# Kernel tuning notes

Hardware: AMD Instinct MI355X
Metric: run time of the kernel (lower is better)

The kernel has to match this reference:

```python
import jax, jax.numpy as jnp
import numpy as np
from jax import lax

B, T, D = 8, 4096, 1024


def setup_inputs() -> dict:
    key = jax.random.key(0)
    ks = jax.random.split(key, 8)
    s = 1.0 / np.sqrt(D)  # keep GEMM outputs O(1)
    return {
        "x": jax.random.normal(ks[0], (B, T, D), dtype=jnp.float32),
        "state_p": jnp.zeros((B, D), dtype=jnp.float32),
        "decay": 0.8 + 0.19 * jax.random.uniform(ks[1], (D,), dtype=jnp.float32),  # ~0.9, stable
        "mass": jnp.ones((D,), dtype=jnp.float32),
        "Wq": s * jax.random.normal(ks[2], (D, D), dtype=jnp.float32),
        "bq": jnp.zeros((D,), dtype=jnp.float32),
        "Wk": s * jax.random.normal(ks[3], (D, D), dtype=jnp.float32),
        "bk": jnp.zeros((D,), dtype=jnp.float32),
        "Wv": s * jax.random.normal(ks[4], (D, D), dtype=jnp.float32),
        "bv": jnp.zeros((D,), dtype=jnp.float32),
    }


def reference(x, state_p, decay, mass, Wq, bq, Wk, bk, Wv, bv):
    # Batch all per-timestep projections into single GEMMs over (B*T) tokens.
    k_logit = jnp.einsum("btd,ed->bte", x, Wk) + bk        # [B,T,D]
    v = jnp.einsum("btd,ed->bte", x, Wv) + bv              # [B,T,D]
    u = jax.nn.sigmoid(k_logit) * v                          # gated input, [B,T,D]

    # Diagonal linear recurrence p_t = decay * p_{t-1} + u_t via scan over time.
    def step(p, u_t):
        p = p * decay + u_t
        return p, p

    final_p, ps = lax.scan(step, state_p, jnp.swapaxes(u, 0, 1))  # ps: [T,B,D]
    p = jnp.swapaxes(ps, 0, 1)                                     # [B,T,D]

    velocities = (jnp.einsum("btd,ed->bte", p, Wq) + bq) / mass    # [B,T,D]
    return velocities, final_p
```

## Files before the change

### kernel.cpp

```cpp
#include <hip/hip_runtime.h>
#include <stdint.h>
#include <stddef.h>

#define D_DIM 1024
#define T_LEN 4096
#define B_SZ 8
#define M_ROWS 32768
#define KTOT 1024
#define CHUNK 64
#define NCHUNK 64

typedef unsigned short u16;
typedef unsigned short u16x8 __attribute__((ext_vector_type(8)));
typedef __bf16 bf16x8 __attribute__((ext_vector_type(8)));
typedef float f32x4 __attribute__((ext_vector_type(4)));

__device__ __forceinline__ u16 f2bf(float f) {
    union { float f; unsigned u; } v; v.f = f;
    unsigned r = v.u + 0x7fffu + ((v.u >> 16) & 1u);
    return (u16)(r >> 16);
}
__device__ __forceinline__ float bf2f(u16 h) {
    union { unsigned u; float f; } v; v.u = ((unsigned)h) << 16;
    return v.f;
}

__global__ void convert_all_kernel(const float* __restrict__ x,
                                   const float* __restrict__ Wk, const float* __restrict__ Wv,
                                   const float* __restrict__ Wq,
                                   u16* __restrict__ xb, u16* __restrict__ wcat,
                                   u16* __restrict__ wqb) {
    const int NX = (M_ROWS * D_DIM) / 4;
    const int total = NX + 3072 * 256;
    int stride = gridDim.x * blockDim.x;
    for (int j = blockIdx.x * blockDim.x + threadIdx.x; j < total; j += stride) {
        const float4* s4;
        ushort4* d4;
        if (j < NX) {
            s4 = (const float4*)x + j;
            d4 = (ushort4*)xb + j;
        } else {
            int idx = j - NX;
            int r = idx >> 8, c4 = idx & 255;
            if (r < 2048) {
                int g = r >> 5, jj = r & 31;
                s4 = (const float4*)((jj < 16 ? Wk : Wv) + (size_t)(g * 16 + (jj & 15)) * D_DIM) + c4;
                d4 = (ushort4*)(wcat + (size_t)r * D_DIM) + c4;
            } else {
                s4 = (const float4*)(Wq + (size_t)(r - 2048) * D_DIM) + c4;
                d4 = (ushort4*)(wqb + (size_t)(r - 2048) * D_DIM) + c4;
            }
        }
        float4 v = *s4;
        ushort4 o;
        o.x = f2bf(v.x); o.y = f2bf(v.y); o.z = f2bf(v.z); o.w = f2bf(v.w);
        *d4 = o;
    }
}

__device__ __forceinline__ void gload16(const u16* g, u16* l) {
    __builtin_amdgcn_global_load_lds(
        (const __attribute__((address_space(1))) void*)g,
        (__attribute__((address_space(3))) void*)l,
        16, 0, 0);
}

template<bool CAT>
__global__ __launch_bounds__(512, 2) void gemm18_kernel(
    const u16* __restrict__ A,
    const u16* __restrict__ Bg,
    const float* __restrict__ bias0,
    const float* __restrict__ bias1,
    u16* __restrict__ Uout,
    float* __restrict__ Fout,
    const float* __restrict__ decay,
    float* __restrict__ localc)
{
    constexpr int NT = KTOT / 64;
    __shared__ u16 smem[2 * 32768];

    const int tid  = threadIdx.x;
    const int w    = tid >> 6;
    const int lane = tid & 63;

    const int cpx = gridDim.x >> 3;
    const int swz = (blockIdx.x & 7) * cpx + (blockIdx.x >> 3);
    const int nCol = CAT ? 8 : 4;
    const int M0 = (swz / nCol) * 256;
    const int N0 = (swz % nCol) * 256;

    const int srow = lane >> 2;
    const int sg   = (lane & 3) ^ ((srow >> 1) & 3);

    const u16* pA0 = A  + (size_t)(M0 + w * 32 +      srow) * KTOT + sg * 8;
    const u16* pA1 = A  + (size_t)(M0 + w * 32 + 16 + srow) * KTOT + sg * 8;
    const u16* pB0 = Bg + (size_t)(N0 + w * 32 +      srow) * KTOT + sg * 8;
    const u16* pB1 = Bg + (size_t)(N0 + w * 32 + 16 + srow) * KTOT + sg * 8;

    auto stA = [&](u16* nxt, int h) {
        gload16(pA0, nxt + h * 8192 + w * 1024);       pA0 += 32;
        gload16(pA1, nxt + h * 8192 + w * 1024 + 512); pA1 += 32;
    };
    auto stB = [&](u16* nxt, int h) {
        gload16(pB0, nxt + 16384 + h * 8192 + w * 1024);       pB0 += 32;
        gload16(pB1, nxt + 16384 + h * 8192 + w * 1024 + 512); pB1 += 32;
    };

    const int wrow = (w >> 2) * 128;
    const int wcol = (w & 3) * 64;
    const int fr = lane & 15;
    const int fq = lane >> 4;

    int offA[8], offB[4];
#pragma unroll
    for (int m = 0; m < 8; ++m) {
        int row = wrow + m * 16 + fr;
        offA[m] = row * 32 + ((fq ^ ((row >> 1) & 3)) << 3);
    }
#pragma unroll
    for (int n = 0; n < 4; ++n) {
        int row = wcol + n * 16 + fr;
        offB[n] = 16384 + row * 32 + ((fq ^ ((row >> 1) & 3)) << 3);
    }

    f32x4 acc[8][4] = {};
    bf16x8 aA[4], aB[4], aC[4], aD[4], bA[4], bC[4];

    stA(smem, 0); stB(smem, 0); stA(smem, 1); stB(smem, 1);
    asm volatile("s_waitcnt vmcnt(4)" ::: "memory");
    __builtin_amdgcn_s_barrier();
#pragma unroll
    for (int m = 0; m < 4; ++m) aA[m] = *(const bf16x8*)(smem + offA[m]);
#pragma unroll
    for (int n = 0; n < 4; ++n) bA[n] = *(const bf16x8*)(smem + offB[n]);

#pragma unroll 1
    for (int t = 0; t < NT; ++t) {
        const u16* cur = smem + (t & 1) * 32768;
        u16* nxt = smem + ((t + 1) & 1) * 32768;
        const bool pf = (t + 1 < NT);

#pragma unroll
        for (int m = 0; m < 4; ++m) aB[m] = *(const bf16x8*)(cur + offA[4 + m]);
        if (pf) stA(nxt, 0);
#pragma unroll
        for (int m = 0; m < 4; ++m)
#pragma unroll
            for (int n = 0; n < 4; ++n)
                acc[m][n] = __builtin_amdgcn_mfma_f32_16x16x32_bf16(aA[m], bA[n], acc[m][n], 0, 0, 0);

        if (pf) { asm volatile("s_waitcnt vmcnt(2)" ::: "memory"); }
        else    { asm volatile("s_waitcnt vmcnt(0)" ::: "memory"); }
        __builtin_amdgcn_s_barrier();
#pragma unroll
        for (int m = 0; m < 4; ++m) aC[m] = *(const bf16x8*)(cur + 8192 + offA[m]);
#pragma unroll
        for (int n = 0; n < 4; ++n) bC[n] = *(const bf16x8*)(cur + 8192 + offB[n]);
        if (pf) stB(nxt, 0);
#pragma unroll
        for (int m = 0; m < 4; ++m)
#pragma unroll
            for (int n = 0; n < 4; ++n)
                acc[4 + m][n] = __builtin_amdgcn_mfma_f32_16x16x32_bf16(aB[m], bA[n], acc[4 + m][n], 0, 0, 0);

#pragma unroll
        for (int m = 0; m < 4; ++m) aD[m] = *(const bf16x8*)(cur + 8192 + offA[4 + m]);
        if (pf) stA(nxt, 1);
#pragma unroll
        for (int m = 0; m < 4; ++m)
#pragma unroll
            for (int n = 0; n < 4; ++n)
                acc[m][n] = __builtin_amdgcn_mfma_f32_16x16x32_bf16(aC[m], bC[n], acc[m][n], 0, 0, 0);

        if (pf) { asm volatile("s_waitcnt vmcnt(2)" ::: "memory"); }
        __builtin_amdgcn_s_barrier();
        if (pf) {
#pragma unroll
            for (int m = 0; m < 4; ++m) aA[m] = *(const bf16x8*)(nxt + offA[m]);
#pragma unroll
            for (int n = 0; n < 4; ++n) bA[n] = *(const bf16x8*)(nxt + offB[n]);
            stB(nxt, 1);
        }
#pragma unroll
        for (int m = 0; m < 4; ++m)
#pragma unroll
            for (int n = 0; n < 4; ++n)
                acc[4 + m][n] = __builtin_amdgcn_mfma_f32_16x16x32_bf16(aD[m], bC[n], acc[4 + m][n], 0, 0, 0);
    }

    if (CAT) {
        asm volatile("s_waitcnt lgkmcnt(0) vmcnt(0)" ::: "memory");
        __syncthreads();
        u16 (*uld)[128] = (u16(*)[128])smem;
        const int ucol0 = N0 / 2;
#pragma unroll
        for (int m = 0; m < 8; ++m) {
#pragma unroll
            for (int p = 0; p < 2; ++p) {
                int lcol = (w & 3) * 32 + p * 16 + fr;
                float b0 = bias0[ucol0 + lcol];
                float b1 = bias1[ucol0 + lcol];
#pragma unroll
                for (int j = 0; j < 4; ++j) {
                    int row = wrow + m * 16 + fq * 4 + j;
                    float kl = acc[m][2 * p][j] + b0;
                    float vv = acc[m][2 * p + 1][j] + b1;
                    float sig = 1.0f / (1.0f + __expf(-kl));
                    uld[row][lcol ^ (((row >> 2) & 3) << 4)] = f2bf(sig * vv);
                }
            }
        }
        __syncthreads();
#pragma unroll
        for (int g = 0; g < 8; ++g) {
            int idx = tid + g * 512;
            int row = idx >> 4, grp = idx & 15;
            int lcol = (grp * 8) ^ (((row >> 2) & 3) << 4);
            *(u16x8*)(Uout + (size_t)(M0 + row) * D_DIM + ucol0 + grp * 8) =
                *(const u16x8*)&uld[row][lcol];
        }
        {
            int chunk = tid >> 7;
            int col   = tid & 127;
            float dec = decay[ucol0 + col];
            float carry = 0.f;
#pragma unroll 4
            for (int s = 0; s < 64; ++s) {
                int r = chunk * 64 + s;
                carry = fmaf(carry, dec, bf2f(uld[r][col ^ (((r >> 2) & 3) << 4)]));
            }
            localc[(size_t)(M0 / 64 + chunk) * D_DIM + ucol0 + col] = carry;
        }
    } else {
#pragma unroll
        for (int n = 0; n < 4; ++n) {
            int col = N0 + wcol + n * 16 + fr;
            float b0 = bias0[col];
            float b1 = bias1[col];
#pragma unroll
            for (int m = 0; m < 8; ++m) {
                int row0 = M0 + wrow + m * 16 + fq * 4;
#pragma unroll
                for (int j = 0; j < 4; ++j)
                    Fout[(size_t)(row0 + j) * D_DIM + col] = (acc[m][n][j] + b0) / b1;
            }
        }
    }
}

__global__ __launch_bounds__(1024) void carry_scan_kernel(
    const float* __restrict__ localc, const float* __restrict__ state_p,
    const float* __restrict__ decay, float* __restrict__ prefix,
    float* __restrict__ final_p)
{
    __shared__ float Vs[64][17], Gs[64][17];
    const int tid = threadIdx.x;
    const int c  = tid >> 4;
    const int dl = tid & 15;
    const int b  = blockIdx.x >> 6;
    const int dg = blockIdx.x & 63;
    const int d  = dg * 16 + dl;

    float dec = decay[d];
    float g = dec;
#pragma unroll
    for (int i = 0; i < 6; ++i) g *= g;
    float v = localc[(size_t)(b * NCHUNK + c) * D_DIM + d];
    Vs[c][dl] = v; Gs[c][dl] = g;
    __syncthreads();
#pragma unroll
    for (int s = 1; s < 64; s <<= 1) {
        float lv = 0.f, lg = 1.f;
        if (c >= s) { lv = Vs[c - s][dl]; lg = Gs[c - s][dl]; }
        __syncthreads();
        if (c >= s) {
            float sv = Vs[c][dl], sgg = Gs[c][dl];
            Vs[c][dl] = fmaf(lv, sgg, sv);
            Gs[c][dl] = lg * sgg;
        }
        __syncthreads();
    }
    float P0 = state_p[b * D_DIM + d];
    float pref = (c == 0) ? P0 : fmaf(P0, Gs[c - 1][dl], Vs[c - 1][dl]);
    prefix[(size_t)(b * NCHUNK + c) * D_DIM + d] = pref;
    if (c == 63)
        final_p[b * D_DIM + d] = fmaf(P0, Gs[63][dl], Vs[63][dl]);
}

__global__ void reconstruct_kernel(u16* __restrict__ u, const float* __restrict__ decay,
                                   const float* __restrict__ prefix) {
    int id = blockIdx.x * blockDim.x + threadIdx.x;
    int d8 = id & 127;
    int c  = (id >> 7) & (NCHUNK - 1);
    int b  = id >> 13;
    float4 dlo = ((const float4*)decay)[d8 * 2];
    float4 dhi = ((const float4*)decay)[d8 * 2 + 1];
    float dec[8] = {dlo.x, dlo.y, dlo.z, dlo.w, dhi.x, dhi.y, dhi.z, dhi.w};
    const float* pf = prefix + ((size_t)(b * NCHUNK + c)) * D_DIM + d8 * 8;
    float p[8];
#pragma unroll
    for (int j = 0; j < 8; ++j) p[j] = pf[j];
    u16* up = u + ((size_t)b * T_LEN + (size_t)c * CHUNK) * D_DIM + d8 * 8;
    for (int s = 0; s < CHUNK; ++s) {
        u16x8 v = *(const u16x8*)(up + (size_t)s * D_DIM);
        u16x8 o;
#pragma unroll
        for (int j = 0; j < 8; ++j) {
            p[j] = fmaf(p[j], dec[j], bf2f(v[j]));
            o[j] = f2bf(p[j]);
        }
        *(u16x8*)(up + (size_t)s * D_DIM) = o;
    }
}

extern "C" void kernel_launch(void* const* d_in, const int* in_sizes, int n_in,
                              void* d_out, int out_size, void* d_ws, size_t ws_size,
                              hipStream_t stream) {
    const float* x       = (const float*)d_in[0];
    const float* state_p = (const float*)d_in[1];
    const float* decay   = (const float*)d_in[2];
    const float* mass    = (const float*)d_in[3];
    const float* Wq      = (const float*)d_in[4];
    const float* bq      = (const float*)d_in[5];
    const float* Wk      = (const float*)d_in[6];
    const float* bk      = (const float*)d_in[7];
    const float* Wv      = (const float*)d_in[8];
    const float* bv      = (const float*)d_in[9];

    float* out     = (float*)d_out;
    float* final_p = out + (size_t)M_ROWS * D_DIM;

    u16* xb = (u16*)d_out;

    u16* wcat = (u16*)d_ws;
    u16* wqb  = wcat + 2048 * 1024;
    u16* ub   = wqb + 1024 * 1024;
    float* localc = (float*)(ub + (size_t)M_ROWS * D_DIM);
    float* prefix = localc + B_SZ * NCHUNK * D_DIM;

    convert_all_kernel<<<4096, 256, 0, stream>>>(x, Wk, Wv, Wq, xb, wcat, wqb);

    gemm18_kernel<true><<<dim3(1024), dim3(512), 0, stream>>>(
        xb, wcat, bk, bv, ub, nullptr, decay, localc);

    carry_scan_kernel<<<512, 1024, 0, stream>>>(localc, state_p, decay, prefix, final_p);
    reconstruct_kernel<<<256, 256, 0, stream>>>(ub, decay, prefix);

    gemm18_kernel<false><<<dim3(512), dim3(512), 0, stream>>>(
        ub, wqb, bq, mass, nullptr, out, nullptr, nullptr);
}
```

Before: 291.7 us.

## Split final Wq GEMM into dedicated 256x128-tile kernel with 1024 blocks

```diff
diff --git a/kernel.cpp b/kernel.cpp
--- a/kernel.cpp
+++ b/kernel.cpp
@@ -65,14 +65,12 @@
         16, 0, 0);
 }
 
-template<bool CAT>
-__global__ __launch_bounds__(512, 2) void gemm18_kernel(
+__global__ __launch_bounds__(512, 2) void gemm_cat_kernel(
     const u16* __restrict__ A,
     const u16* __restrict__ Bg,
     const float* __restrict__ bias0,
     const float* __restrict__ bias1,
     u16* __restrict__ Uout,
-    float* __restrict__ Fout,
     const float* __restrict__ decay,
     float* __restrict__ localc)
 {
@@ -85,9 +83,8 @@
 
     const int cpx = gridDim.x >> 3;
     const int swz = (blockIdx.x & 7) * cpx + (blockIdx.x >> 3);
-    const int nCol = CAT ? 8 : 4;
-    const int M0 = (swz / nCol) * 256;
-    const int N0 = (swz % nCol) * 256;
+    const int M0 = (swz >> 3) * 256;
+    const int N0 = (swz & 7) * 256;
 
     const int srow = lane >> 2;
     const int sg   = (lane & 3) ^ ((srow >> 1) & 3);
@@ -107,7 +104,6 @@
     };
 
     const int wrow = (w >> 2) * 128;
-    const int wcol = (w & 3) * 64;
     const int fr = lane & 15;
     const int fq = lane >> 4;
 
@@ -119,7 +115,7 @@
     }
 #pragma unroll
     for (int n = 0; n < 4; ++n) {
-        int row = wcol + n * 16 + fr;
+        int row = (w & 3) * 64 + n * 16 + fr;
         offB[n] = 16384 + row * 32 + ((fq ^ ((row >> 1) & 3)) << 3);
     }
 
@@ -188,62 +184,149 @@
                 acc[4 + m][n] = __builtin_amdgcn_mfma_f32_16x16x32_bf16(aD[m], bC[n], acc[4 + m][n], 0, 0, 0);
     }
 
-    if (CAT) {
-        asm volatile("s_waitcnt lgkmcnt(0) vmcnt(0)" ::: "memory");
-        __syncthreads();
-        u16 (*uld)[128] = (u16(*)[128])smem;
-        const int ucol0 = N0 / 2;
-#pragma unroll
-        for (int m = 0; m < 8; ++m) {
-#pragma unroll
-            for (int p = 0; p < 2; ++p) {
-                int lcol = (w & 3) * 32 + p * 16 + fr;
-                float b0 = bias0[ucol0 + lcol];
-                float b1 = bias1[ucol0 + lcol];
-#pragma unroll
-                for (int j = 0; j < 4; ++j) {
-                    int row = wrow + m * 16 + fq * 4 + j;
-                    float kl = acc[m][2 * p][j] + b0;
-                    float vv = acc[m][2 * p + 1][j] + b1;
-                    float sig = 1.0f / (1.0f + __expf(-kl));
-                    uld[row][lcol ^ (((row >> 2) & 3) << 4)] = f2bf(sig * vv);
-                }
+    asm volatile("s_waitcnt lgkmcnt(0) vmcnt(0)" ::: "memory");
+    __syncthreads();
+
+    u16 (*uld)[128] = (u16(*)[128])smem;
+    const int ucol0 = N0 / 2;
+#pragma unroll
+    for (int m = 0; m < 8; ++m) {
+#pragma unroll
+        for (int p = 0; p < 2; ++p) {
+            int lcol = (w & 3) * 32 + p * 16 + fr;
+            float b0 = bias0[ucol0 + lcol];
+            float b1 = bias1[ucol0 + lcol];
+#pragma unroll
+            for (int j = 0; j < 4; ++j) {
+                int row = wrow + m * 16 + fq * 4 + j;
+                float kl = acc[m][2 * p][j] + b0;
+                float vv = acc[m][2 * p + 1][j] + b1;
+                float sig = 1.0f / (1.0f + __expf(-kl));
+                uld[row][lcol ^ (((row >> 2) & 3) << 4)] = f2bf(sig * vv);
             }
         }
-        __syncthreads();
-#pragma unroll
-        for (int g = 0; g < 8; ++g) {
-            int idx = tid + g * 512;
-            int row = idx >> 4, grp = idx & 15;
-            int lcol = (grp * 8) ^ (((row >> 2) & 3) << 4);
-            *(u16x8*)(Uout + (size_t)(M0 + row) * D_DIM + ucol0 + grp * 8) =
-                *(const u16x8*)&uld[row][lcol];
-        }
-        {
-            int chunk = tid >> 7;
-            int col   = tid & 127;
-            float dec = decay[ucol0 + col];
-            float carry = 0.f;
+    }
+    __syncthreads();
+#pragma unroll
+    for (int g = 0; g < 8; ++g) {
+        int idx = tid + g * 512;
+        int row = idx >> 4, grp = idx & 15;
+        int lcol = (grp * 8) ^ (((row >> 2) & 3) << 4);
+        *(u16x8*)(Uout + (size_t)(M0 + row) * D_DIM + ucol0 + grp * 8) =
+            *(const u16x8*)&uld[row][lcol];
+    }
+    {
+        int chunk = tid >> 7;
+        int col   = tid & 127;
+        float dec = decay[ucol0 + col];
+        float carry = 0.f;
 #pragma unroll 4
-            for (int s = 0; s < 64; ++s) {
-                int r = chunk * 64 + s;
-                carry = fmaf(carry, dec, bf2f(uld[r][col ^ (((r >> 2) & 3) << 4)]));
-            }
-            localc[(size_t)(M0 / 64 + chunk) * D_DIM + ucol0 + col] = carry;
-        }
-    } else {
-#pragma unroll
-        for (int n = 0; n < 4; ++n) {
-            int col = N0 + wcol + n * 16 + fr;
-            float b0 = bias0[col];
-            float b1 = bias1[col];
-#pragma unroll
-            for (int m = 0; m < 8; ++m) {
-                int row0 = M0 + wrow + m * 16 + fq * 4;
-#pragma unroll
-                for (int j = 0; j < 4; ++j)
-                    Fout[(size_t)(row0 + j) * D_DIM + col] = (acc[m][n][j] + b0) / b1;
-            }
+        for (int s = 0; s < 64; ++s) {
+            int r = chunk * 64 + s;
+            carry = fmaf(carry, dec, bf2f(uld[r][col ^ (((r >> 2) & 3) << 4)]));
+        }
+        localc[(size_t)(M0 / 64 + chunk) * D_DIM + ucol0 + col] = carry;
+    }
+}
+
+__global__ __launch_bounds__(512, 2) void gemm_single_kernel(
+    const u16* __restrict__ A,
+    const u16* __restrict__ Bg,
+    const float* __restrict__ bias0,
+    const float* __restrict__ bias1,
+    float* __restrict__ Fout)
+{
+    constexpr int NT = KTOT / 32;
+    __shared__ u16 smem[2 * 12288];
+
+    const int tid  = threadIdx.x;
+    const int w    = tid >> 6;
+    const int lane = tid & 63;
+
+    const int cpx = gridDim.x >> 3;
+    const int swz = (blockIdx.x & 7) * cpx + (blockIdx.x >> 3);
+    const int M0 = (swz >> 3) * 256;
+    const int N0 = (swz & 7) * 128;
+
+    const int srow = lane >> 2;
+    const int sg   = (lane & 3) ^ ((srow >> 1) & 3);
+
+    const u16* pA0 = A  + (size_t)(M0 + w * 32 +      srow) * KTOT + sg * 8;
+    const u16* pA1 = A  + (size_t)(M0 + w * 32 + 16 + srow) * KTOT + sg * 8;
+    const u16* pB  = Bg + (size_t)(N0 + w * 16 +      srow) * KTOT + sg * 8;
+
+    auto stage = [&](int buf) {
+        u16* s = smem + buf * 12288;
+        gload16(pA0, s + w * 1024);        pA0 += 32;
+        gload16(pA1, s + w * 1024 + 512);  pA1 += 32;
+        gload16(pB,  s + 8192 + w * 512);  pB  += 32;
+    };
+
+    const int wrow = (w >> 1) * 64;
+    const int wcol = (w & 1) * 64;
+    const int fr = lane & 15;
+    const int fq = lane >> 4;
+
+    int offA[4], offB[4];
+#pragma unroll
+    for (int m = 0; m < 4; ++m) {
+        int row = wrow + m * 16 + fr;
+        offA[m] = row * 32 + ((fq ^ ((row >> 1) & 3)) << 3);
+    }
+#pragma unroll
+    for (int n = 0; n < 4; ++n) {
+        int row = wcol + n * 16 + fr;
+        offB[n] = 8192 + row * 32 + ((fq ^ ((row >> 1) & 3)) << 3);
+    }
+
+    f32x4 acc[4][4] = {};
+    bf16x8 aP[4], bP[4], aQ[4], bQ[4];
+
+    stage(0); stage(1);
+    asm volatile("s_waitcnt vmcnt(3)" ::: "memory");
+    __builtin_amdgcn_s_barrier();
+#pragma unroll
+    for (int m = 0; m < 4; ++m) aP[m] = *(const bf16x8*)(smem + offA[m]);
+#pragma unroll
+    for (int n = 0; n < 4; ++n) bP[n] = *(const bf16x8*)(smem + offB[n]);
+
+#define SUBTILE(S, AC, BC, AN, BN_)                                                  \
+  {                                                                                  \
+    const int s_ = (S);                                                              \
+    asm volatile("s_waitcnt vmcnt(0) lgkmcnt(0)" ::: "memory");                      \
+    __builtin_amdgcn_s_barrier();                                                    \
+    __builtin_amdgcn_sched_barrier(0);                                               \
+    if (s_ + 2 < NT) stage(s_ & 1);                                                  \
+    if (s_ + 1 < NT) {                                                               \
+      const u16* nb_ = smem + ((s_ + 1) & 1) * 12288;                                \
+      _Pragma("unroll") for (int m = 0; m < 4; ++m)                                  \
+        AN[m] = *(const bf16x8*)(nb_ + offA[m]);                                     \
+      _Pragma("unroll") for (int n = 0; n < 4; ++n)                                  \
+        BN_[n] = *(const bf16x8*)(nb_ + offB[n]);                                    \
+    }                                                                                \
+    _Pragma("unroll") for (int m = 0; m < 4; ++m)                                    \
+      _Pragma("unroll") for (int n = 0; n < 4; ++n)                                  \
+        acc[m][n] = __builtin_amdgcn_mfma_f32_16x16x32_bf16(AC[m], BC[n], acc[m][n], 0, 0, 0); \
+  }
+
+#pragma unroll 1
+    for (int s = 0; s < NT; s += 2) {
+        SUBTILE(s,     aP, bP, aQ, bQ);
+        SUBTILE(s + 1, aQ, bQ, aP, bP);
+    }
+#undef SUBTILE
+
+#pragma unroll
+    for (int n = 0; n < 4; ++n) {
+        int col = N0 + wcol + n * 16 + fr;
+        float b0 = bias0[col];
+        float b1 = bias1[col];
+#pragma unroll
+        for (int m = 0; m < 4; ++m) {
+            int row0 = M0 + wrow + m * 16 + fq * 4;
+#pragma unroll
+            for (int j = 0; j < 4; ++j)
+                Fout[(size_t)(row0 + j) * D_DIM + col] = (acc[m][n][j] + b0) / b1;
         }
     }
 }
@@ -340,12 +423,12 @@
 
     convert_all_kernel<<<4096, 256, 0, stream>>>(x, Wk, Wv, Wq, xb, wcat, wqb);
 
-    gemm18_kernel<true><<<dim3(1024), dim3(512), 0, stream>>>(
-        xb, wcat, bk, bv, ub, nullptr, decay, localc);
+    gemm_cat_kernel<<<dim3(1024), dim3(512), 0, stream>>>(
+        xb, wcat, bk, bv, ub, decay, localc);
 
     carry_scan_kernel<<<512, 1024, 0, stream>>>(localc, state_p, decay, prefix, final_p);
     reconstruct_kernel<<<256, 256, 0, stream>>>(ub, decay, prefix);
 
-    gemm18_kernel<false><<<dim3(512), dim3(512), 0, stream>>>(
-        ub, wqb, bq, mass, nullptr, out, nullptr, nullptr);
-}
+    gemm_single_kernel<<<dim3(1024), dim3(512), 0, stream>>>(
+        ub, wqb, bq, mass, out);
+}
```

Result: slower. 318.1 us (+9.0%).
